# Performance work log

Hardware: AMD Instinct MI355X
Metric: run time of the kernel (lower is better)

## Reference

```python
import jax, jax.numpy as jnp
import numpy as np

DIM = 1024
HEADS = 16
DH = DIM // HEADS          # 64
ROT_DIM = 2 * DH           # 128, rotary applied over concatenated x/a head dim
B, N = 2, 2048


def l2norm(t, eps=1e-12):
    # F.normalize(p=2, dim=-1)
    n = jnp.sqrt(jnp.sum(t * t, axis=-1, keepdims=True))
    return t / jnp.maximum(n, eps)


def rotate_half(t):
    t1, t2 = jnp.split(t, 2, axis=-1)
    return jnp.concatenate([-t2, t1], axis=-1)


def apply_rotary(q, k):
    # q: [b,h,n,ROT_DIM], k: [b,1,n,ROT_DIM]
    n = q.shape[-2]
    inv_freq = 1.0 / (10000.0 ** (jnp.arange(0, ROT_DIM, 2, dtype=jnp.float32) / ROT_DIM))
    freqs = jnp.outer(jnp.arange(n, dtype=jnp.float32), inv_freq)  # [n, ROT_DIM/2]
    emb = jnp.concatenate([freqs, freqs], axis=-1)                 # [n, ROT_DIM]
    cos, sin = jnp.cos(emb), jnp.sin(emb)
    q = q * cos + rotate_half(q) * sin
    k = k * cos + rotate_half(k) * sin
    return q, k


def setup_inputs() -> dict:
    key = jax.random.key(0)
    ks = jax.random.split(key, 6)
    s = 0.02
    return {
        "x": jax.random.normal(ks[0], (B, N, DIM), jnp.float32),
        "a": jax.random.normal(ks[1], (B, N, DIM), jnp.float32),
        "Wq_x": jax.random.normal(ks[2], (DIM, DIM), jnp.float32) * s,
        "Wkv_x": jax.random.normal(ks[3], (2 * DH, DIM), jnp.float32) * s,
        "Wq_a": jax.random.normal(ks[4], (DIM, DIM), jnp.float32) * s,
        "Wkv_a": jax.random.normal(ks[5], (2 * DH, DIM), jnp.float32) * s,
        "qx_scale": jnp.ones((HEADS, 1, DH), jnp.float32),
        "qa_scale": jnp.ones((HEADS, 1, DH), jnp.float32),
        "kx_scale": jnp.ones((1, 1, DH), jnp.float32),
        "ka_scale": jnp.ones((1, 1, DH), jnp.float32),
    }


def reference(x, a, Wq_x, Wkv_x, Wq_a, Wkv_a, qx_scale, qa_scale, kx_scale, ka_scale):
    b, n, _ = x.shape
    # q projections: [b,n,dim] -> [b,h,n,dh]
    q_x = (x @ Wq_x.T).reshape(b, n, HEADS, DH).transpose(0, 2, 1, 3)
    q_a = (a @ Wq_a.T).reshape(b, n, HEADS, DH).transpose(0, 2, 1, 3)
    # shared single KV head: [b,n,2*dh] -> two [b,1,n,dh]
    kv_x = x @ Wkv_x.T
    k_x, v_x = jnp.split(kv_x[:, None], 2, axis=-1)
    kv_a = a @ Wkv_a.T
    k_a, v_a = jnp.split(kv_a[:, None], 2, axis=-1)
    # qk-norm with learned per-head (q) / shared (k) scales
    q_x = l2norm(q_x) * qx_scale
    q_a = l2norm(q_a) * qa_scale
    k_x = l2norm(k_x) * kx_scale
    k_a = l2norm(k_a) * ka_scale
    # concat modalities along feature dim -> head dim 2*dh
    q = jnp.concatenate([q_x, q_a], axis=-1)   # [b,h,n,2dh]
    k = jnp.concatenate([k_x, k_a], axis=-1)   # [b,1,n,2dh]
    v = jnp.concatenate([v_x, v_a], axis=-1)   # [b,1,n,2dh]
    q, k = apply_rotary(q, k)
    # SDPA with broadcasted single KV head
    scale = 1.0 / jnp.sqrt(jnp.float32(ROT_DIM))
    k2, v2 = k[:, 0], v[:, 0]                  # [b,n,2dh]
    scores = jnp.einsum("bhqd,bkd->bhqk", q * scale, k2)
    attn = jax.nn.softmax(scores, axis=-1)
    out = jnp.einsum("bhqk,bkd->bhqd", attn, v2)  # [b,h,n,2dh]
    return out.transpose(0, 2, 1, 3).reshape(b, n, HEADS * ROT_DIM)
```

## Files before the change

### kernel.cpp

```cpp
#include <hip/hip_runtime.h>
#include <math.h>

#define DIM   1024
#define HEADS 16
#define DH    64
#define ROT   128
#define BATCH 2
#define SEQ   2048
#define ROWS  (BATCH*SEQ)
#define PCOLS (DIM + 2*DH)
#define ASCALE 0.08838834764831845f

typedef short bf16x8 __attribute__((ext_vector_type(8)));
typedef float f32x16 __attribute__((ext_vector_type(16)));

static __device__ __forceinline__ unsigned short f2bf(float f) {
    union { float f; unsigned u; } v; v.f = f;
    unsigned r = v.u + 0x7fffu + ((v.u >> 16) & 1u);
    return (unsigned short)(r >> 16);
}
static __device__ __forceinline__ float bf2f(unsigned short u) {
    union { unsigned u; float f; } v; v.u = (unsigned)u << 16;
    return v.f;
}

#define GL2LDS(gp, lp) __builtin_amdgcn_global_load_lds(                    \
    (const __attribute__((address_space(1))) void*)(gp),                    \
    (__attribute__((address_space(3))) void*)(lp), 16, 0, 0)
#define CFENCE() asm volatile("" ::: "memory")
#define WAIT_VM8()  __builtin_amdgcn_s_waitcnt(0xF78)
#define WAIT_VM0()  __builtin_amdgcn_s_waitcnt(0xF70)

__global__ __launch_bounds__(256) void convert_kernel(
    const float* __restrict__ x, const float* __restrict__ a,
    const float* __restrict__ Wq_x, const float* __restrict__ Wkv_x,
    const float* __restrict__ Wq_a, const float* __restrict__ Wkv_a,
    unsigned short* __restrict__ xbf, unsigned short* __restrict__ wbf,
    float2* __restrict__ tbl)
{
    const int blk = blockIdx.x;
    const float LN1E4_64 = 0.14391156831213f;
    if (blk >= 2624) {
        int local = blk - 2624;
        int pos = local * 16 + (threadIdx.x >> 4);
        int i   = threadIdx.x & 15;
        #pragma unroll
        for (int j = 0; j < 4; j++) {
            int jd = i * 4 + j;
            float th = (float)pos * expf(-LN1E4_64 * (float)jd);
            float sn, cs; sincosf(th, &sn, &cs);
            tbl[pos * 64 + jd] = make_float2(cs, sn);
        }
        return;
    }
    const float* s; unsigned short* d; int seg0;
    if      (blk < 1024) { s = x;     d = xbf;           seg0 = 0;    }
    else if (blk < 2048) { s = a;     d = xbf + 4194304; seg0 = 1024; }
    else if (blk < 2304) { s = Wq_x;  d = wbf;           seg0 = 2048; }
    else if (blk < 2336) { s = Wkv_x; d = wbf + 1048576; seg0 = 2304; }
    else if (blk < 2592) { s = Wq_a;  d = wbf + 1179648; seg0 = 2336; }
    else                 { s = Wkv_a; d = wbf + 2228224; seg0 = 2592; }
    long lb = ((long)blk - seg0) * 1024;
    #pragma unroll
    for (int j = 0; j < 4; j++) {
        long idx = lb + j * 256 + threadIdx.x;
        float4 v = ((const float4*)s)[idx];
        ((ushort4*)d)[idx] = make_ushort4(f2bf(v.x), f2bf(v.y), f2bf(v.z), f2bf(v.w));
    }
}

__global__ __launch_bounds__(256) void mfma_gemm_kernel(
    const unsigned short* __restrict__ xbf, const unsigned short* __restrict__ wbf,
    unsigned short* __restrict__ Pbf)
{
    const int mt = blockIdx.x, jt = blockIdx.y, side = blockIdx.z;
    const unsigned short* Ag = xbf + ((size_t)side * ROWS  + mt * 128) * DIM;
    const unsigned short* Bg = wbf + ((size_t)side * PCOLS + jt * 128) * DIM;
    unsigned short* Pp = Pbf + (size_t)side * ROWS * PCOLS;

    __shared__ __align__(16) unsigned short As[128 * 32];
    __shared__ __align__(16) unsigned short Bs[128 * 32];

    const int tid  = threadIdx.x;
    const int wave = tid >> 6, lane = tid & 63;
    const int m = lane & 31, hl = lane >> 5;
    const int wr = wave >> 1, wc = wave & 1;

    f32x16 acc[2][2];
    #pragma unroll
    for (int i2 = 0; i2 < 2; i2++)
        #pragma unroll
        for (int j2 = 0; j2 < 2; j2++) acc[i2][j2] = 0.0f;

    int sr[2], sg[2]; unsigned ldsb[2];
    #pragma unroll
    for (int it = 0; it < 2; it++) {
        int s = it * 256 + tid;
        sr[it] = s >> 2;
        sg[it] = (s & 3) ^ ((sr[it] >> 1) & 3);
        ldsb[it] = (unsigned)(it * 256 + wave * 64) * 16;
    }

    for (int k0 = 0; k0 < DIM; k0 += 32) {
        __syncthreads();
        #pragma unroll
        for (int it = 0; it < 2; it++) {
            GL2LDS(Ag + (size_t)sr[it] * DIM + k0 + sg[it] * 8, (char*)As + ldsb[it]);
            GL2LDS(Bg + (size_t)sr[it] * DIM + k0 + sg[it] * 8, (char*)Bs + ldsb[it]);
        }
        __syncthreads();
        #pragma unroll
        for (int kp = 0; kp < 2; kp++) {
            bf16x8 af[2], bff[2];
            #pragma unroll
            for (int t2 = 0; t2 < 2; t2++) {
                int ra = wr * 64 + t2 * 32 + m;
                int ga = (kp * 2 + hl) ^ ((ra >> 1) & 3);
                af[t2] = *(const bf16x8*)&As[ra * 32 + ga * 8];
                int rb = wc * 64 + t2 * 32 + m;
                int gb = (kp * 2 + hl) ^ ((rb >> 1) & 3);
                bff[t2] = *(const bf16x8*)&Bs[rb * 32 + gb * 8];
            }
            #pragma unroll
            for (int i2 = 0; i2 < 2; i2++)
                #pragma unroll
                for (int j2 = 0; j2 < 2; j2++)
                    acc[i2][j2] = __builtin_amdgcn_mfma_f32_32x32x16_bf16(
                        af[i2], bff[j2], acc[i2][j2], 0, 0, 0);
        }
    }

    const int m0 = mt * 128 + wr * 64;
    const int n0 = jt * 128 + wc * 64;
    #pragma unroll
    for (int i2 = 0; i2 < 2; i2++)
        #pragma unroll
        for (int j2 = 0; j2 < 2; j2++)
            #pragma unroll
            for (int r = 0; r < 16; r++) {
                int row = m0 + i2 * 32 + (r & 3) + 8 * (r >> 2) + 4 * hl;
                int col = n0 + j2 * 32 + m;
                Pp[(size_t)row * PCOLS + col] = f2bf(acc[i2][j2][r]);
            }
}

__global__ __launch_bounds__(256) void fuse_kernel(
    const unsigned short* __restrict__ Pbf,
    const float* __restrict__ qx_scale, const float* __restrict__ qa_scale,
    const float* __restrict__ kx_scale, const float* __restrict__ ka_scale,
    const float2* __restrict__ tbl,
    unsigned short* __restrict__ qbuf, unsigned short* __restrict__ kbuf,
    unsigned short* __restrict__ vbufT)
{
    const int row = blockIdx.x;
    const int b = row >> 11, pos = row & 2047;
    const unsigned short* Px = Pbf + (size_t)row * PCOLS;
    const unsigned short* Pa = Pbf + (size_t)ROWS * PCOLS + (size_t)row * PCOLS;
    const int tid = threadIdx.x;
    const int h = tid >> 4, i = tid & 15;
    const float2* tb = tbl + pos * 64;

    ushort4 xu = *(const ushort4*)(Px + h * DH + i * 4);
    ushort4 au = *(const ushort4*)(Pa + h * DH + i * 4);
    float xr[4] = {bf2f(xu.x), bf2f(xu.y), bf2f(xu.z), bf2f(xu.w)};
    float ar[4] = {bf2f(au.x), bf2f(au.y), bf2f(au.z), bf2f(au.w)};
    float ssx = xr[0]*xr[0] + xr[1]*xr[1] + xr[2]*xr[2] + xr[3]*xr[3];
    float ssa = ar[0]*ar[0] + ar[1]*ar[1] + ar[2]*ar[2] + ar[3]*ar[3];
    #pragma unroll
    for (int off = 1; off < 16; off <<= 1) {
        ssx += __shfl_xor(ssx, off, 16);
        ssa += __shfl_xor(ssa, off, 16);
    }
    float inx = 1.0f / fmaxf(sqrtf(ssx), 1e-12f);
    float ina = 1.0f / fmaxf(sqrtf(ssa), 1e-12f);
    unsigned short qlo[4], qhi[4];
    #pragma unroll
    for (int j = 0; j < 4; j++) {
        int jd = i * 4 + j;
        float qx = xr[j] * inx * qx_scale[h * DH + jd];
        float qa = ar[j] * ina * qa_scale[h * DH + jd];
        float2 cssn = tb[jd];
        qlo[j] = f2bf((qx * cssn.x - qa * cssn.y) * ASCALE);
        qhi[j] = f2bf((qa * cssn.x + qx * cssn.y) * ASCALE);
    }
    unsigned short* qp = qbuf + (((size_t)(b * HEADS + h)) * SEQ + pos) * ROT;
    *(ushort4*)(qp + i * 4)      = make_ushort4(qlo[0], qlo[1], qlo[2], qlo[3]);
    *(ushort4*)(qp + DH + i * 4) = make_ushort4(qhi[0], qhi[1], qhi[2], qhi[3]);

    if (tid < 16) {
        ushort4 kxu = *(const ushort4*)(Px + DIM + tid * 4);
        ushort4 kau = *(const ushort4*)(Pa + DIM + tid * 4);
        float kxr[4] = {bf2f(kxu.x), bf2f(kxu.y), bf2f(kxu.z), bf2f(kxu.w)};
        float kar[4] = {bf2f(kau.x), bf2f(kau.y), bf2f(kau.z), bf2f(kau.w)};
        float sx = kxr[0]*kxr[0] + kxr[1]*kxr[1] + kxr[2]*kxr[2] + kxr[3]*kxr[3];
        float sa = kar[0]*kar[0] + kar[1]*kar[1] + kar[2]*kar[2] + kar[3]*kar[3];
        #pragma unroll
        for (int off = 1; off < 16; off <<= 1) {
            sx += __shfl_xor(sx, off, 16);
            sa += __shfl_xor(sa, off, 16);
        }
        float ikx = 1.0f / fmaxf(sqrtf(sx), 1e-12f);
        float ika = 1.0f / fmaxf(sqrtf(sa), 1e-12f);
        unsigned short klo[4], khi[4];
        #pragma unroll
        for (int j = 0; j < 4; j++) {
            int jd = tid * 4 + j;
            float kx = kxr[j] * ikx * kx_scale[jd];
            float ka = kar[j] * ika * ka_scale[jd];
            float2 cssn = tb[jd];
            klo[j] = f2bf(kx * cssn.x - ka * cssn.y);
            khi[j] = f2bf(ka * cssn.x + kx * cssn.y);
        }
        unsigned short* kp = kbuf + ((size_t)b * SEQ + pos) * ROT;
        *(ushort4*)(kp + tid * 4)      = make_ushort4(klo[0], klo[1], klo[2], klo[3]);
        *(ushort4*)(kp + DH + tid * 4) = make_ushort4(khi[0], khi[1], khi[2], khi[3]);
    }
    if (tid >= 64 && tid < 96) {
        int iv = tid - 64;
        unsigned short* vT = vbufT + (size_t)b * ROT * SEQ + pos;
        const unsigned short* src; int d;
        if (iv < 16) { src = Px + DIM + DH + iv * 4;        d = iv * 4;              }
        else         { src = Pa + DIM + DH + (iv - 16) * 4; d = DH + (iv - 16) * 4;  }
        ushort4 v4 = *(const ushort4*)src;
        vT[(size_t)(d + 0) * SEQ] = v4.x;
        vT[(size_t)(d + 1) * SEQ] = v4.y;
        vT[(size_t)(d + 2) * SEQ] = v4.z;
        vT[(size_t)(d + 3) * SEQ] = v4.w;
    }
}

__global__ __launch_bounds__(256, 2) void attn_kernel(
    const unsigned short* __restrict__ qbuf,
    const unsigned short* __restrict__ kbuf,
    const unsigned short* __restrict__ vbufT,
    float* __restrict__ out)
{
    const int qb = blockIdx.x, h = blockIdx.y, b = blockIdx.z;
    __shared__ __align__(16) unsigned short Ks[2][64 * 128];
    __shared__ __align__(16) unsigned short Vs[2][128 * 64];
    const int tid  = threadIdx.x;
    const int wave = tid >> 6, lane = tid & 63;
    const int m = lane & 31, hl = lane >> 5;
    const int q0 = qb * 128 + wave * 32;

    bf16x8 qf[8];
    {
        const unsigned short* qp = qbuf + (((size_t)(b * HEADS + h)) * SEQ + q0 + m) * ROT + hl * 8;
        #pragma unroll
        for (int c = 0; c < 8; c++) qf[c] = *(const bf16x8*)(qp + c * 16);
    }

    f32x16 oacc[4];
    #pragma unroll
    for (int dt = 0; dt < 4; dt++) oacc[dt] = 0.0f;
    float lsum = 0.f;

    const unsigned short* kb_ = kbuf  + (size_t)b * SEQ * ROT;
    const unsigned short* vb_ = vbufT + (size_t)b * ROT * SEQ;

    const unsigned short* ksrc[4];
    const unsigned short* vsrc[4];
    unsigned ldsoff[4];
    #pragma unroll
    for (int i = 0; i < 4; i++) {
        int fg = i * 256 + tid;
        int krow = fg >> 4, kg = fg & 15;
        ksrc[i] = kb_ + (size_t)krow * ROT + ((kg ^ (krow & 15)) << 3);
        int rv = fg >> 3, gv = fg & 7;
        vsrc[i] = vb_ + (size_t)rv * SEQ + ((gv ^ (rv & 7)) << 3);
        ldsoff[i] = (unsigned)(i * 256 + wave * 64) * 16;
    }

    #pragma unroll
    for (int i = 0; i < 4; i++) {
        GL2LDS(ksrc[i], (char*)Ks[0] + ldsoff[i]);
        GL2LDS(vsrc[i], (char*)Vs[0] + ldsoff[i]);
    }

    for (int t = 0; t < 32; t++) {
        const int buf = t & 1;
        if (t < 31) {
            #pragma unroll
            for (int i = 0; i < 4; i++) {
                GL2LDS(ksrc[i] + (size_t)(t + 1) * 64 * ROT, (char*)Ks[buf ^ 1] + ldsoff[i]);
                GL2LDS(vsrc[i] + (t + 1) * 64,               (char*)Vs[buf ^ 1] + ldsoff[i]);
            }
        }
        CFENCE();
        if (t < 31) WAIT_VM8(); else WAIT_VM0();
        __builtin_amdgcn_s_barrier();
        CFENCE();

        #pragma unroll
        for (int kg = 0; kg < 2; kg++) {
            f32x16 st = 0.0f;
            #pragma unroll
            for (int c = 0; c < 8; c++) {
                bf16x8 af = *(const bf16x8*)&Ks[buf][(kg * 32 + m) * 128 +
                                                     (((2 * c + hl) ^ (m & 15)) << 3)];
                st = __builtin_amdgcn_mfma_f32_32x32x16_bf16(af, qf[c], st, 0, 0, 0);
            }
            float p[16];
            #pragma unroll
            for (int r = 0; r < 16; r++) { p[r] = __expf(st[r]); lsum += p[r]; }

            #pragma unroll
            for (int w = 0; w < 2; w++) {
                float pj[8];
                #pragma unroll
                for (int tq = 0; tq < 4; tq++) {
                    float send = hl ? p[8 * w + tq]     : p[8 * w + 4 + tq];
                    float own  = hl ? p[8 * w + 4 + tq] : p[8 * w + tq];
                    float recv = __shfl_xor(send, 32);
                    pj[tq]     = hl ? recv : own;
                    pj[4 + tq] = hl ? own  : recv;
                }
                bf16x8 aP;
                #pragma unroll
                for (int j = 0; j < 8; j++) aP[j] = (short)f2bf(pj[j]);
                #pragma unroll
                for (int dt = 0; dt < 4; dt++) {
                    int d = dt * 32 + m;
                    bf16x8 vf = *(const bf16x8*)&Vs[buf][d * 64 +
                                                         (((kg * 4 + w * 2 + hl) ^ (d & 7)) << 3)];
                    oacc[dt] = __builtin_amdgcn_mfma_f32_32x32x16_bf16(aP, vf, oacc[dt], 0, 0, 0);
                }
            }
        }

        CFENCE();
        __builtin_amdgcn_s_barrier();
        CFENCE();
    }

    lsum += __shfl_xor(lsum, 32);
    float* ob = out + ((size_t)(b * SEQ + q0)) * (HEADS * ROT) + h * ROT + m;
    #pragma unroll
    for (int r = 0; r < 16; r++) {
        int qrow = (r & 3) + 8 * (r >> 2) + 4 * hl;
        float linv = 1.0f / __shfl(lsum, qrow);
        float* orow = ob + (size_t)qrow * (HEADS * ROT);
        #pragma unroll
        for (int dt = 0; dt < 4; dt++) orow[dt * 32] = oacc[dt][r] * linv;
    }
}

extern "C" void kernel_launch(void* const* d_in, const int* in_sizes, int n_in,
                              void* d_out, int out_size, void* d_ws, size_t ws_size,
                              hipStream_t stream) {
    (void)in_sizes; (void)n_in; (void)out_size; (void)ws_size;
    const float* x        = (const float*)d_in[0];
    const float* a        = (const float*)d_in[1];
    const float* Wq_x     = (const float*)d_in[2];
    const float* Wkv_x    = (const float*)d_in[3];
    const float* Wq_a     = (const float*)d_in[4];
    const float* Wkv_a    = (const float*)d_in[5];
    const float* qx_scale = (const float*)d_in[6];
    const float* qa_scale = (const float*)d_in[7];
    const float* kx_scale = (const float*)d_in[8];
    const float* ka_scale = (const float*)d_in[9];
    float* out = (float*)d_out;

    unsigned short* Pbf   = (unsigned short*)d_ws;
    unsigned short* qbuf  = Pbf   + (size_t)2 * ROWS * PCOLS;
    unsigned short* kbuf  = qbuf  + (size_t)BATCH * HEADS * SEQ * ROT;
    unsigned short* vbufT = kbuf  + (size_t)BATCH * SEQ * ROT;
    unsigned short* xbf   = vbufT + (size_t)BATCH * SEQ * ROT;
    unsigned short* wbf   = xbf   + (size_t)2 * ROWS * DIM;
    float2*         tbl   = (float2*)(wbf + (size_t)2 * PCOLS * DIM);

    convert_kernel<<<dim3(2752), 256, 0, stream>>>(x, a, Wq_x, Wkv_x, Wq_a, Wkv_a,
                                                   xbf, wbf, tbl);
    mfma_gemm_kernel<<<dim3(32, 9, 2), 256, 0, stream>>>(xbf, wbf, Pbf);
    fuse_kernel<<<dim3(ROWS), 256, 0, stream>>>(Pbf, qx_scale, qa_scale, kx_scale, ka_scale,
                                                tbl, qbuf, kbuf, vbufT);
    attn_kernel<<<dim3(SEQ / 128, HEADS, BATCH), 256, 0, stream>>>(qbuf, kbuf, vbufT, out);
}
```

Baseline: 233.0 us.

## Use exp2 with folded log2e, packed bf16 cvt, permlane32 swap, V swizzle, setprio

Folds log2(e) into the attention scale so softmax can use the native exp2 instruction instead of __expf. Replaces the per-element shuffle exchange and software bf16 rounding with packed v_cvt_pk_bf16_f32 conversions and permlane32_swap. Changes the V tile LDS XOR swizzle to use (d>>2)&7, aiming to reduce bank conflicts. Raises wave priority around the MFMA blocks to improve interleaving across waves. The new swizzle has to stay consistent between the global-to-LDS writes and the reads, and the swap ordering has to match the MFMA A-operand layout.

Measured after the change: 222.3 us. 1.05x faster.

```diff
diff --git a/kernel.cpp b/kernel.cpp
--- a/kernel.cpp
+++ b/kernel.cpp
@@ -9,10 +9,11 @@
 #define SEQ   2048
 #define ROWS  (BATCH*SEQ)
 #define PCOLS (DIM + 2*DH)
-#define ASCALE 0.08838834764831845f
+#define ASCALE (0.08838834764831845f * 1.4426950408889634f)
 
 typedef short bf16x8 __attribute__((ext_vector_type(8)));
 typedef float f32x16 __attribute__((ext_vector_type(16)));
+typedef unsigned u32x2 __attribute__((ext_vector_type(2)));
 
 static __device__ __forceinline__ unsigned short f2bf(float f) {
     union { float f; unsigned u; } v; v.f = f;
@@ -267,7 +268,7 @@
         int krow = fg >> 4, kg = fg & 15;
         ksrc[i] = kb_ + (size_t)krow * ROT + ((kg ^ (krow & 15)) << 3);
         int rv = fg >> 3, gv = fg & 7;
-        vsrc[i] = vb_ + (size_t)rv * SEQ + ((gv ^ (rv & 7)) << 3);
+        vsrc[i] = vb_ + (size_t)rv * SEQ + ((gv ^ ((rv >> 2) & 7)) << 3);
         ldsoff[i] = (unsigned)(i * 256 + wave * 64) * 16;
     }
 
@@ -294,37 +295,41 @@
         #pragma unroll
         for (int kg = 0; kg < 2; kg++) {
             f32x16 st = 0.0f;
+            __builtin_amdgcn_s_setprio(1);
             #pragma unroll
             for (int c = 0; c < 8; c++) {
                 bf16x8 af = *(const bf16x8*)&Ks[buf][(kg * 32 + m) * 128 +
                                                      (((2 * c + hl) ^ (m & 15)) << 3)];
                 st = __builtin_amdgcn_mfma_f32_32x32x16_bf16(af, qf[c], st, 0, 0, 0);
             }
+            __builtin_amdgcn_s_setprio(0);
+
             float p[16];
             #pragma unroll
-            for (int r = 0; r < 16; r++) { p[r] = __expf(st[r]); lsum += p[r]; }
+            for (int r = 0; r < 16; r++) { p[r] = __builtin_amdgcn_exp2f(st[r]); lsum += p[r]; }
 
             #pragma unroll
             for (int w = 0; w < 2; w++) {
-                float pj[8];
-                #pragma unroll
-                for (int tq = 0; tq < 4; tq++) {
-                    float send = hl ? p[8 * w + tq]     : p[8 * w + 4 + tq];
-                    float own  = hl ? p[8 * w + 4 + tq] : p[8 * w + tq];
-                    float recv = __shfl_xor(send, 32);
-                    pj[tq]     = hl ? recv : own;
-                    pj[4 + tq] = hl ? own  : recv;
-                }
-                bf16x8 aP;
-                #pragma unroll
-                for (int j = 0; j < 8; j++) aP[j] = (short)f2bf(pj[j]);
+                unsigned pk0, pk1, pk2, pk3;
+                asm("v_cvt_pk_bf16_f32 %0, %1, %2" : "=v"(pk0) : "v"(p[8*w+0]), "v"(p[8*w+1]));
+                asm("v_cvt_pk_bf16_f32 %0, %1, %2" : "=v"(pk1) : "v"(p[8*w+2]), "v"(p[8*w+3]));
+                asm("v_cvt_pk_bf16_f32 %0, %1, %2" : "=v"(pk2) : "v"(p[8*w+4]), "v"(p[8*w+5]));
+                asm("v_cvt_pk_bf16_f32 %0, %1, %2" : "=v"(pk3) : "v"(p[8*w+6]), "v"(p[8*w+7]));
+                u32x2 s0 = __builtin_amdgcn_permlane32_swap(pk0, pk2, false, false);
+                u32x2 s1 = __builtin_amdgcn_permlane32_swap(pk1, pk3, false, false);
+                union { unsigned u[4]; bf16x8 v; } apu;
+                apu.u[0] = s0[0]; apu.u[1] = s1[0]; apu.u[2] = s0[1]; apu.u[3] = s1[1];
+                bf16x8 aP = apu.v;
+
+                __builtin_amdgcn_s_setprio(1);
                 #pragma unroll
                 for (int dt = 0; dt < 4; dt++) {
                     int d = dt * 32 + m;
                     bf16x8 vf = *(const bf16x8*)&Vs[buf][d * 64 +
-                                                         (((kg * 4 + w * 2 + hl) ^ (d & 7)) << 3)];
+                                 (((kg * 4 + w * 2 + hl) ^ ((d >> 2) & 7)) << 3)];
                     oacc[dt] = __builtin_amdgcn_mfma_f32_32x32x16_bf16(aP, vf, oacc[dt], 0, 0, 0);
                 }
+                __builtin_amdgcn_s_setprio(0);
             }
         }
 
```
